# Kernel optimization log

Measured on AMD Instinct MI355X. Metric: run time of the kernel, lower is better.

The kernel has to match this reference:

```python
import jax, jax.numpy as jnp
import numpy as np

jax.config.update("jax_enable_x64", True)  # original uses complex128 FFTs

MS_H, MS_W, MS_D = 10, 10, 2
EPS = 1e-08


def _window_mean(x, wx, wy, wz):
    """Mean over all (wx,wy,wz) VALID windows of 3D x, via a summed-area table.
    Equivalent math to tf.nn.avg_pool3d(stride 1, VALID)."""
    X, Y, Z = x.shape
    A, B, C = X - wx + 1, Y - wy + 1, Z - wz + 1  # (2*MS_W+1, 2*MS_H+1, 2*MS_D+1)
    S = jnp.pad(jnp.cumsum(jnp.cumsum(jnp.cumsum(x, 0), 1), 2), ((1, 0), (1, 0), (1, 0)))
    g = lambda ox, oy, oz: jax.lax.dynamic_slice(S, (ox, oy, oz), (A, B, C))
    ws = (g(wx, wy, wz) - g(0, wy, wz) - g(wx, 0, wz) - g(wx, wy, 0)
          + g(0, 0, wz) + g(0, wy, 0) + g(wx, 0, 0) - g(0, 0, 0))
    return ws / float(wx * wy * wz)


def _forward(fr, template):
    # fr: (1, X, Y, Z, 1) float32; template: (X, Y, Z, 1) float32
    tpl = template[..., 0]                       # (X, Y, Z)
    X, Y, Z = tpl.shape
    # --- normalize_template ---
    tpl_zm = tpl - jnp.mean(tpl)
    tpl_var = jnp.sum(jnp.square(tpl_zm)) + EPS  # scalar
    target_freq = jnp.fft.fftn(tpl_zm.astype(jnp.complex128), axes=(0, 1, 2))
    # --- normalize_image ---
    img = fr[0, ..., 0]                          # (X, Y, Z)
    imgs_zm = img - jnp.mean(img)
    wx, wy, wz = X - 2 * MS_W, Y - 2 * MS_H, Z - 2 * MS_D
    m1 = _window_mean(img, wx, wy, wz)           # avg_pool3d of img
    m2 = _window_mean(jnp.square(img), wx, wy, wz)
    shp_prod = float(X * Y * Z)
    imgs_var = m2 - jnp.square(m1) / shp_prod + EPS
    imgs_var = jnp.where(imgs_var < 0, jnp.zeros_like(imgs_var), imgs_var)
    denominator = jnp.sqrt(tpl_var * imgs_var)   # (21, 21, 5)
    # --- FFT cross-correlation ---
    fr_freq = jnp.fft.fftn(imgs_zm.astype(jnp.complex128), axes=(0, 1, 2))
    cc = jnp.abs(jnp.fft.ifftn(fr_freq * jnp.conj(target_freq), axes=(0, 1, 2))).astype(jnp.float32)
    mx, my, mz = X // 2, Y // 2, Z // 2
    rolled_cc = jnp.roll(cc, (mx, my, mz), axis=(0, 1, 2))
    ncc = rolled_cc[mx - MS_W:mx + MS_W + 1,
                    my - MS_H:my + MS_H + 1,
                    mz - MS_D:mz + MS_D + 1] / denominator.astype(jnp.float32)
    ncc = jnp.where(jnp.isnan(ncc), jnp.zeros_like(ncc), ncc)
    # --- argmax_3d + Gaussian subpixel refine ---
    A, B, C = ncc.shape
    flat_idx = jnp.argmax(ncc.reshape(-1))
    sx = flat_idx // (B * C)
    sy = (flat_idx % (B * C)) // C
    sz = flat_idx - sx * (B * C) - C * sy
    ncc_log = jnp.log(ncc)
    v = lambda dx, dy, dz: ncc_log[sx + dx, sy + dy, sz + dz]
    six = 6.0 * v(0, 0, 0)
    sh_x = (-(sx - MS_H)).astype(jnp.float32) - (v(-1, 0, 0) - v(1, 0, 0)) / (2 * v(-1, 0, 0) - six + 2 * v(1, 0, 0))
    sh_y = (-(sy - MS_W)).astype(jnp.float32) - (v(0, -1, 0) - v(0, 1, 0)) / (2 * v(0, -1, 0) - six + 2 * v(0, 1, 0))
    sh_z = (-(sz - MS_D)).astype(jnp.float32) - (v(0, 0, -1) - v(0, 0, 1)) / (2 * v(0, 0, -1) - six + 2 * v(0, 0, 1))
    return (sh_x.reshape(1, 1), sh_y.reshape(1, 1), sh_z.reshape(1, 1),
            rolled_cc[None, ..., None], ncc[None, ..., None])


def setup_inputs() -> dict:
    key = jax.random.key(0)
    k1, k2 = jax.random.split(key)
    X, Y, Z = 512, 512, 32
    base = jax.random.normal(k1, (X, Y, Z), dtype=jnp.float32)
    # box-smooth so the NCC has a broad positive peak (log-interp stays finite)
    sm = base
    for ax in range(3):
        sm = sum(jnp.roll(sm, s, ax) for s in (-2, -1, 0, 1, 2)) / 5.0
    template = sm[..., None]
    fr = (jnp.roll(sm, (3, -2, 1), axis=(0, 1, 2))
          + 0.02 * jax.random.normal(k2, (X, Y, Z), dtype=jnp.float32))[None, ..., None]
    return {"fr": fr, "template": template}


def reference(fr, template):
    return _forward(fr, template)
```

## Files before the change

kernel.cpp:

```cpp
#include <hip/hip_runtime.h>
#include <hip/hip_bf16.h>
#include <math.h>


#define NTOT 8388608
#define NLINES 262144
#define OUT_ROLL_OFF 3
#define OUT_NCC_OFF 8388611
#define WIN_PROD 6777792.0
#define EPSV 1e-8

#define WS_HC_OFF 0UL
#define WS_ZS1_OFF 0UL
#define WS_ZS2_OFF 10485760UL
#define WS_YS1_OFF 20971520UL
#define WS_YS2_OFF 21401600UL
#define WS_PART_OFF 31457280UL
#define WS_DENOM_OFF 134217728UL

typedef float2 cf;
__device__ __forceinline__ cf cfadd(cf a, cf b){ return make_float2(a.x+b.x, a.y+b.y); }
__device__ __forceinline__ cf cfsub(cf a, cf b){ return make_float2(a.x-b.x, a.y-b.y); }
__device__ __forceinline__ cf cfmul(cf a, cf b){ return make_float2(a.x*b.x-a.y*b.y, a.x*b.y+a.y*b.x); }
__device__ __forceinline__ cf cfnegi(cf a){ return make_float2(a.y, -a.x); }
__device__ __forceinline__ cf cfposi(cf a){ return make_float2(-a.y, a.x); }

#define RT2F 0.70710678118654752440f
__device__ __forceinline__ cf cw64f(cf v){ return make_float2(RT2F*(v.x+v.y), RT2F*(v.y-v.x)); }
__device__ __forceinline__ cf cw192f(cf v){ return make_float2(RT2F*(v.y-v.x), -RT2F*(v.x+v.y)); }
__device__ __forceinline__ cf cw64i(cf v){ return make_float2(RT2F*(v.x-v.y), RT2F*(v.x+v.y)); }
__device__ __forceinline__ cf cw192i(cf v){ return make_float2(-RT2F*(v.x+v.y), RT2F*(v.x-v.y)); }

#define SKW(i) ((i) + ((i) >> 3))
#define LROW 580

template <int H>
__device__ __forceinline__ void fwd_r4(cf* ln, const cf* tw, int lane) {
    const int MUL2 = 256 / (2 * H);
#pragma unroll
    for (int g = 0; g < 2; ++g) {
        int j = lane + 64 * g;
        int t = j & (H - 1);
        int i0 = ((j & ~(H - 1)) << 2) + t;
        cf A = ln[SKW(i0)];
        cf B = ln[SKW(i0 + H)];
        cf C = ln[SKW(i0 + 2 * H)];
        cf D = ln[SKW(i0 + 3 * H)];
        cf w1 = tw[t * MUL2];
        cf w2 = make_float2(w1.x * w1.x - w1.y * w1.y, 2.0f * w1.x * w1.y);
        cf u = cfadd(A, C), v = cfadd(B, D);
        cf p = cfmul(cfsub(A, C), w1);
        cf q = cfnegi(cfmul(cfsub(B, D), w1));
        ln[SKW(i0)]         = cfadd(u, v);
        ln[SKW(i0 + H)]     = cfmul(cfsub(u, v), w2);
        ln[SKW(i0 + 2 * H)] = cfadd(p, q);
        ln[SKW(i0 + 3 * H)] = cfmul(cfsub(p, q), w2);
    }
}

template <int H>
__device__ __forceinline__ void inv_r4(cf* ln, const cf* tw, int lane) {
    const int MUL2 = 256 / (2 * H);
#pragma unroll
    for (int g = 0; g < 2; ++g) {
        int j = lane + 64 * g;
        int t = j & (H - 1);
        int i0 = ((j & ~(H - 1)) << 2) + t;
        cf A = ln[SKW(i0)];
        cf B = ln[SKW(i0 + H)];
        cf C = ln[SKW(i0 + 2 * H)];
        cf D = ln[SKW(i0 + 3 * H)];
        cf tww = tw[t * MUL2];
        cf w2 = make_float2(tww.x, -tww.y);
        cf wH = make_float2(w2.x * w2.x - w2.y * w2.y, 2.0f * w2.x * w2.y);
        cf vb = cfmul(B, wH), vd = cfmul(D, wH);
        cf a0 = cfadd(A, vb), a1 = cfsub(A, vb);
        cf c0 = cfadd(C, vd), c1 = cfsub(C, vd);
        cf t0 = cfmul(c0, w2);
        cf t1 = cfposi(cfmul(c1, w2));
        ln[SKW(i0)]         = cfadd(a0, t0);
        ln[SKW(i0 + 2 * H)] = cfsub(a0, t0);
        ln[SKW(i0 + H)]     = cfadd(a1, t1);
        ln[SKW(i0 + 3 * H)] = cfsub(a1, t1);
    }
}

__device__ __forceinline__ void fwd_r8(cf* ln, int lane) {
    cf* rp = ln + 9 * lane;
    cf L0 = rp[0], L1 = rp[1], L2 = rp[2], L3 = rp[3];
    cf L4 = rp[4], L5 = rp[5], L6 = rp[6], L7 = rp[7];
    cf s0 = cfadd(L0, L4), d0 = cfsub(L0, L4);
    cf s1 = cfadd(L1, L5), d1 = cw64f(cfsub(L1, L5));
    cf s2 = cfadd(L2, L6), d2 = cfnegi(cfsub(L2, L6));
    cf s3 = cfadd(L3, L7), d3 = cw192f(cfsub(L3, L7));
    cf e0 = cfadd(s0, s2), e2 = cfsub(s0, s2);
    cf e1 = cfadd(s1, s3), e3 = cfnegi(cfsub(s1, s3));
    cf f0 = cfadd(d0, d2), f2 = cfsub(d0, d2);
    cf f1 = cfadd(d1, d3), f3 = cfnegi(cfsub(d1, d3));
    rp[0] = cfadd(e0, e1); rp[1] = cfsub(e0, e1);
    rp[2] = cfadd(e2, e3); rp[3] = cfsub(e2, e3);
    rp[4] = cfadd(f0, f1); rp[5] = cfsub(f0, f1);
    rp[6] = cfadd(f2, f3); rp[7] = cfsub(f2, f3);
}

__device__ __forceinline__ void inv_r8(cf* ln, int lane) {
    cf* rp = ln + 9 * lane;
    cf L0 = rp[0], L1 = rp[1], L2 = rp[2], L3 = rp[3];
    cf L4 = rp[4], L5 = rp[5], L6 = rp[6], L7 = rp[7];
    cf a0 = cfadd(L0, L1), a1 = cfsub(L0, L1), a2 = cfadd(L2, L3), a3 = cfsub(L2, L3);
    cf a4 = cfadd(L4, L5), a5 = cfsub(L4, L5), a6 = cfadd(L6, L7), a7 = cfsub(L6, L7);
    cf b0 = cfadd(a0, a2), b2 = cfsub(a0, a2);
    cf v13 = cfposi(a3);
    cf b1 = cfadd(a1, v13), b3 = cfsub(a1, v13);
    cf b4 = cfadd(a4, a6), b6 = cfsub(a4, a6);
    cf v57 = cfposi(a7);
    cf b5 = cfadd(a5, v57), b7 = cfsub(a5, v57);
    cf v0 = b4, v1 = cw64i(b5), v2 = cfposi(b6), v3 = cw192i(b7);
    rp[0] = cfadd(b0, v0); rp[4] = cfsub(b0, v0);
    rp[1] = cfadd(b1, v1); rp[5] = cfsub(b1, v1);
    rp[2] = cfadd(b2, v2); rp[6] = cfsub(b2, v2);
    rp[3] = cfadd(b3, v3); rp[7] = cfsub(b3, v3);
}

template <int INV>
__device__ __forceinline__ void line_fft512(cf* ln, const cf* tw, int lane) {
    if (!INV) {
        fwd_r4<128>(ln, tw, lane);
        __builtin_amdgcn_wave_barrier();
        fwd_r4<32>(ln, tw, lane);
        __builtin_amdgcn_wave_barrier();
        fwd_r4<8>(ln, tw, lane);
        __builtin_amdgcn_wave_barrier();
        fwd_r8(ln, lane);
    } else {
        inv_r8(ln, lane);
        __builtin_amdgcn_wave_barrier();
        inv_r4<8>(ln, tw, lane);
        __builtin_amdgcn_wave_barrier();
        inv_r4<32>(ln, tw, lane);
        __builtin_amdgcn_wave_barrier();
        inv_r4<128>(ln, tw, lane);
    }
}

static constexpr float W32CF_[16] = {
    1.0f, 0.980785280403230449f, 0.923879532511286756f, 0.831469612302545237f,
    0.707106781186547524f, 0.555570233019602225f, 0.382683432365089772f, 0.195090322016128268f,
    0.0f, -0.195090322016128268f, -0.382683432365089772f, -0.555570233019602225f,
    -0.707106781186547524f, -0.831469612302545237f, -0.923879532511286756f, -0.980785280403230449f};
static constexpr float W32SF_[16] = {
    0.0f, 0.195090322016128268f, 0.382683432365089772f, 0.555570233019602225f,
    0.707106781186547524f, 0.831469612302545237f, 0.923879532511286756f, 0.980785280403230449f,
    1.0f, 0.980785280403230449f, 0.923879532511286756f, 0.831469612302545237f,
    0.707106781186547524f, 0.555570233019602225f, 0.382683432365089772f, 0.195090322016128268f};

template <int INV>
__device__ __forceinline__ void fft32(cf* a) {
    if (INV == 0) {
#pragma unroll
        for (int s = 0; s < 5; ++s) {
            const int h = 16 >> s;
#pragma unroll
            for (int j = 0; j < 16; ++j) {
                const int t = j & (h - 1);
                const int i0 = ((j >> (4 - s)) << (5 - s)) + t;
                const int i1 = i0 + h;
                cf u = a[i0], v = a[i1];
                a[i0] = make_float2(u.x + v.x, u.y + v.y);
                float dx = u.x - v.x, dy = u.y - v.y;
                const float wc = W32CF_[t << s];
                const float ws = -W32SF_[t << s];
                a[i1] = make_float2(dx * wc - dy * ws, dx * ws + dy * wc);
            }
        }
    } else {
#pragma unroll
        for (int s = 0; s < 5; ++s) {
            const int h = 1 << s;
#pragma unroll
            for (int j = 0; j < 16; ++j) {
                const int t = j & (h - 1);
                const int i0 = ((j >> s) << (s + 1)) + t;
                const int i1 = i0 + h;
                const float wc = W32CF_[t << (4 - s)];
                const float ws = W32SF_[t << (4 - s)];
                cf u = a[i0], vr = a[i1];
                cf v = make_float2(vr.x * wc - vr.y * ws, vr.x * ws + vr.y * wc);
                a[i0] = make_float2(u.x + v.x, u.y + v.y);
                a[i1] = make_float2(u.x - v.x, u.y - v.y);
            }
        }
    }
}

__device__ __forceinline__ int mir_br(int b) {
    if (b == 0) return 0;
    int s = 31 - __clz(b);
    return (3 << s) - 1 - b;
}

__global__ __launch_bounds__(256) void k_reduce_tpl(const float4* __restrict__ tpl4,
                                                    double2* __restrict__ part) {
    double st = 0, st2 = 0;
    const int stride = gridDim.x * blockDim.x;
    for (int i = blockIdx.x * blockDim.x + threadIdx.x; i < NTOT / 4; i += stride) {
        float4 t = tpl4[i];
        double t0 = t.x, t1 = t.y, t2 = t.z, t3 = t.w;
        st += t0 + t1 + t2 + t3;
        st2 += t0 * t0 + t1 * t1 + t2 * t2 + t3 * t3;
    }
    __shared__ double s1[256], s2[256];
    int tid = threadIdx.x;
    s1[tid] = st; s2[tid] = st2;
    __syncthreads();
    for (int s = 128; s > 0; s >>= 1) {
        if (tid < s) { s1[tid] += s1[tid + s]; s2[tid] += s2[tid + s]; }
        __syncthreads();
    }
    if (tid == 0) part[blockIdx.x] = make_double2(s1[0], s2[0]);
}

__global__ __launch_bounds__(256) void k_winz(const float* __restrict__ img,
                                              double* __restrict__ zs1,
                                              double* __restrict__ zs2) {
    int line = blockIdx.x * blockDim.x + threadIdx.x;
    long b = (long)line << 5;
    float v[32];
    const float4* p4 = (const float4*)(img + b);
#pragma unroll
    for (int q = 0; q < 8; ++q) {
        float4 f = p4[q];
        v[q * 4 + 0] = f.x; v[q * 4 + 1] = f.y; v[q * 4 + 2] = f.z; v[q * 4 + 3] = f.w;
    }
    double s1 = 0, s2 = 0;
#pragma unroll
    for (int z = 0; z < 28; ++z) {
        double t = (double)v[z];
        s1 += t;
        s2 += t * t;
    }
    long ob = (long)line * 5;
    zs1[ob] = s1; zs2[ob] = s2;
#pragma unroll
    for (int k = 1; k <= 4; ++k) {
        double a = (double)v[27 + k], r = (double)v[k - 1];
        s1 += a - r;
        s2 += a * a - r * r;
        zs1[ob + k] = s1; zs2[ob + k] = s2;
    }
}

__global__ __launch_bounds__(256) void k_winy(const double* __restrict__ zs1,
                                              const double* __restrict__ zs2,
                                              double* __restrict__ ys1,
                                              double* __restrict__ ys2) {
    int t = blockIdx.x * blockDim.x + threadIdx.x;
    if (t >= 2560) return;
    int x = t / 5, c = t % 5;
    long base = (long)x * 512 * 5 + c;
    double s1 = 0, s2 = 0;
    for (int y = 0; y < 492; ++y) {
        s1 += zs1[base + (long)y * 5];
        s2 += zs2[base + (long)y * 5];
    }
    long ob = (long)x * 105 + c;
    ys1[ob] = s1; ys2[ob] = s2;
    for (int k = 1; k <= 20; ++k) {
        s1 += zs1[base + (long)(491 + k) * 5] - zs1[base + (long)(k - 1) * 5];
        s2 += zs2[base + (long)(491 + k) * 5] - zs2[base + (long)(k - 1) * 5];
        ys1[ob + (long)k * 5] = s1;
        ys2[ob + (long)k * 5] = s2;
    }
}

__global__ __launch_bounds__(256) void k_winx_denom(const double* __restrict__ ys1,
                                                    const double* __restrict__ ys2,
                                                    const double2* __restrict__ part,
                                                    float* __restrict__ denom) {
    __shared__ double s1s[256], s2s[256];
    __shared__ double tplvar_s;
    int tid = threadIdx.x;
    {
        double a1 = 0, a2 = 0;
#pragma unroll
        for (int q = 0; q < 4; ++q) {
            double2 p = part[tid + 256 * q];
            a1 += p.x; a2 += p.y;
        }
        s1s[tid] = a1; s2s[tid] = a2;
        __syncthreads();
        for (int s = 128; s > 0; s >>= 1) {
            if (tid < s) { s1s[tid] += s1s[tid + s]; s2s[tid] += s2s[tid + s]; }
            __syncthreads();
        }
        if (tid == 0) {
            double S1 = s1s[0], S2 = s2s[0];
            double mu = S1 / (double)NTOT;
            tplvar_s = S2 - (double)NTOT * mu * mu + EPSV;
        }
        __syncthreads();
    }
    if (tid >= 105) return;
    const double tpl_var = tplvar_s;
    double s1 = 0, s2 = 0;
    for (int x = 0; x < 492; ++x) {
        s1 += ys1[(long)x * 105 + tid];
        s2 += ys2[(long)x * 105 + tid];
    }
    const double wm = 1.0 / WIN_PROD;
    for (int a = 0; a < 21; ++a) {
        double m1 = s1 * wm, m2 = s2 * wm;
        double iv = m2 - (m1 * m1) / (double)NTOT + EPSV;
        if (iv < 0) iv = 0;
        denom[a * 105 + tid] = (float)sqrt(tpl_var * iv);
        if (a < 20) {
            s1 += ys1[(long)(492 + a) * 105 + tid] - ys1[(long)a * 105 + tid];
            s2 += ys2[(long)(492 + a) * 105 + tid] - ys2[(long)a * 105 + tid];
        }
    }
}

__global__ __launch_bounds__(256) void k_pack_fft_z(const float* __restrict__ img,
                                                    const float* __restrict__ tpl,
                                                    cf* __restrict__ d) {
    int line = blockIdx.x * blockDim.x + threadIdx.x;
    long b = (long)line << 5;
    cf a[32];
    const float4* pi4 = (const float4*)(img + b);
    const float4* pt4 = (const float4*)(tpl + b);
#pragma unroll
    for (int q = 0; q < 8; ++q) {
        float4 fi = pi4[q];
        float4 ft = pt4[q];
        a[q * 4 + 0] = make_float2(fi.x, ft.x);
        a[q * 4 + 1] = make_float2(fi.y, ft.y);
        a[q * 4 + 2] = make_float2(fi.z, ft.z);
        a[q * 4 + 3] = make_float2(fi.w, ft.w);
    }
    fft32<0>(a);
#pragma unroll
    for (int z = 0; z < 32; ++z) d[b + z] = a[z];
}

template <int INV>
__global__ __launch_bounds__(1024, 8) void k_fft16(cf* __restrict__ d) {
    __shared__ cf ln[16][LROW];
    __shared__ cf tw[256];
    const int tid = threadIdx.x;
    if (tid < 256) {
        double sv, cv;
        sincos(6.283185307179586476925286766559 * (double)tid / 512.0, &sv, &cv);
        tw[tid] = make_float2((float)cv, (float)(-sv));
    }
    const long base = (long)(blockIdx.x >> 1) * 16384 + (blockIdx.x & 1) * 16;
#pragma unroll
    for (int i = 0; i < 8; ++i) {
        int idx = tid + 1024 * i;
        int lz = idx & 15, e = idx >> 4;
        ln[lz][SKW(e)] = d[base + (long)e * 32 + lz];
    }
    __syncthreads();
    const int c = tid >> 6, lane = tid & 63;
    line_fft512<INV>(ln[c], tw, lane);
    __syncthreads();
#pragma unroll
    for (int i = 0; i < 8; ++i) {
        int idx = tid + 1024 * i;
        int lz = idx & 15, e = idx >> 4;
        d[base + (long)e * 32 + lz] = ln[lz][SKW(e)];
    }
}

__global__ __launch_bounds__(1024, 8) void k_fftx_cross(cf* __restrict__ d) {
    const int bid = blockIdx.x;
    const int y = bid >> 2, tA = bid & 3;
    const int my = mir_br(y);
    const int tB = tA ^ (tA >> 1);
    const int keyA = (y << 2) | tA, keyB = (my << 2) | tB;
    if (keyA > keyB) return;
    const bool dup = (keyA == keyB);

    __shared__ cf ln[16][LROW];
    __shared__ cf tw[256];
    const int tid = threadIdx.x;
    if (tid < 256) {
        double sv, cv;
        sincos(6.283185307179586476925286766559 * (double)tid / 512.0, &sv, &cv);
        tw[tid] = make_float2((float)cv, (float)(-sv));
    }
    const int baseA = y * 32 + tA * 8;
    const int baseB = my * 32 + tB * 8;
#pragma unroll
    for (int i = 0; i < 8; ++i) {
        int idx = tid + 1024 * i;
        int a = idx & 7, half = (idx >> 3) & 1, bx = idx >> 4;
        ln[half * 8 + a][SKW(bx)] = d[(long)bx * 16384 + (half ? baseB : baseA) + a];
    }
    __syncthreads();
    const int c = tid >> 6, lane = tid & 63;
    line_fft512<0>(ln[c], tw, lane);
    __syncthreads();
    const bool dcblk = (bid == 0);
#pragma unroll
    for (int i = 0; i < 4; ++i) {
        int p = tid + 1024 * i;
        int a = p >> 9, bx = p & 511;
        int am = (tA == 0) ? mir_br(a) : 7 - a;
        int mbx = mir_br(bx);
        if (dcblk && p == 0) {
            ln[0][0] = make_float2(0.f, 0.f);
            ln[8][0] = make_float2(0.f, 0.f);
            continue;
        }
        cf h1 = ln[a][SKW(bx)];
        cf h2 = ln[8 + am][SKW(mbx)];
        float Fr = 0.5f * (h1.x + h2.x), Fi = 0.5f * (h1.y - h2.y);
        float Gr = 0.5f * (h1.y + h2.y), Gi = 0.5f * (h2.x - h1.x);
        float Pr = Fr * Gr + Fi * Gi;
        float Pi = Fi * Gr - Fr * Gi;
        ln[a][SKW(bx)] = make_float2(Pr, Pi);
        ln[8 + am][SKW(mbx)] = make_float2(Pr, -Pi);
    }
    __syncthreads();
    line_fft512<1>(ln[c], tw, lane);
    __syncthreads();
#pragma unroll
    for (int i = 0; i < 8; ++i) {
        int idx = tid + 1024 * i;
        int a = idx & 7, half = (idx >> 3) & 1, bx = idx >> 4;
        if (dup && half) continue;
        d[(long)bx * 16384 + (half ? baseB : baseA) + a] = ln[half * 8 + a][SKW(bx)];
    }
}

__global__ __launch_bounds__(256) void k_invz_abs_roll(const cf* __restrict__ d,
                                                       float* __restrict__ out) {
    int line = blockIdx.x * blockDim.x + threadIdx.x;
    int x = line >> 9, y = line & 511;
    long b = (long)line << 5;
    cf a[32];
#pragma unroll
    for (int z = 0; z < 32; ++z) a[z] = d[b + z];
    fft32<1>(a);
    const float invN = 1.0f / 8388608.0f;
    int xo = (x + 256) & 511, yo = (y + 256) & 511;
    long ob = OUT_ROLL_OFF + ((long)(xo << 9 | yo) << 5);
#pragma unroll
    for (int q = 0; q < 8; ++q) {
        int z = q * 4;
        int zo = (z + 16) & 31;
        float4 w;
        w.x = sqrtf(a[z + 0].x * a[z + 0].x + a[z + 0].y * a[z + 0].y) * invN;
        w.y = sqrtf(a[z + 1].x * a[z + 1].x + a[z + 1].y * a[z + 1].y) * invN;
        w.z = sqrtf(a[z + 2].x * a[z + 2].x + a[z + 2].y * a[z + 2].y) * invN;
        w.w = sqrtf(a[z + 3].x * a[z + 3].x + a[z + 3].y * a[z + 3].y) * invN;
        *(float4*)(out + ob + zo) = w;
    }
}

__global__ __launch_bounds__(256) void k_ncc_argmax(const float* __restrict__ denom,
                                                    float* __restrict__ out) {
    __shared__ float sncc[2205];
    __shared__ float bv[256];
    __shared__ int bi[256];
    const int tid = threadIdx.x;
    float best = -INFINITY;
    int bidx = 0x7fffffff;
    for (int i = tid; i < 2205; i += 256) {
        int a = i / 105, r = i % 105;
        int bq = r / 5, cq = r % 5;
        long ridx = OUT_ROLL_OFF + ((long)((246 + a) * 512 + (246 + bq)) << 5) + (14 + cq);
        float v = out[ridx] / denom[i];
        if (isnan(v)) v = 0.f;
        out[OUT_NCC_OFF + i] = v;
        sncc[i] = v;
        if (v > best) { best = v; bidx = i; }
    }
    bv[tid] = best;
    bi[tid] = bidx;
    __syncthreads();
    for (int s = 128; s > 0; s >>= 1) {
        if (tid < s) {
            if (bv[tid + s] > bv[tid] || (bv[tid + s] == bv[tid] && bi[tid + s] < bi[tid])) {
                bv[tid] = bv[tid + s];
                bi[tid] = bi[tid + s];
            }
        }
        __syncthreads();
    }
    if (tid == 0) {
        int idx = bi[0];
        int sx = idx / 105, sy = (idx % 105) / 5, sz = idx % 5;
        auto cl = [](int v, int n) { return v < 0 ? 0 : (v >= n ? n - 1 : v); };
        auto V = [&](int dx, int dy, int dz) {
            return logf(sncc[cl(sx + dx, 21) * 105 + cl(sy + dy, 21) * 5 + cl(sz + dz, 5)]);
        };
        float v0 = V(0, 0, 0);
        float six = 6.0f * v0;
        float am = V(-1, 0, 0), ap = V(1, 0, 0);
        float bm = V(0, -1, 0), bp = V(0, 1, 0);
        float cm = V(0, 0, -1), cp = V(0, 0, 1);
        out[0] = (float)(-(sx - 10)) - (am - ap) / (2.f * am - six + 2.f * ap);
        out[1] = (float)(-(sy - 10)) - (bm - bp) / (2.f * bm - six + 2.f * bp);
        out[2] = (float)(-(sz - 2)) - (cm - cp) / (2.f * cm - six + 2.f * cp);
    }
}

extern "C" void kernel_launch(void* const* d_in, const int* in_sizes, int n_in,
                              void* d_out, int out_size, void* d_ws, size_t ws_size,
                              hipStream_t stream) {
    const float* fr = (const float*)d_in[0];
    const float* tpl = (const float*)d_in[1];
    float* out = (float*)d_out;
    char* ws = (char*)d_ws;

    cf* Hc = (cf*)(ws + WS_HC_OFF);
    double* zs1 = (double*)(ws + WS_ZS1_OFF);
    double* zs2 = (double*)(ws + WS_ZS2_OFF);
    double* ys1 = (double*)(ws + WS_YS1_OFF);
    double* ys2 = (double*)(ws + WS_YS2_OFF);
    double2* part = (double2*)(ws + WS_PART_OFF);
    float* denom = (float*)(ws + WS_DENOM_OFF);

    k_reduce_tpl<<<1024, 256, 0, stream>>>((const float4*)tpl, part);
    k_winz<<<NLINES / 256, 256, 0, stream>>>(fr, zs1, zs2);
    k_winy<<<10, 256, 0, stream>>>(zs1, zs2, ys1, ys2);
    k_winx_denom<<<1, 256, 0, stream>>>(ys1, ys2, part, denom);

    k_pack_fft_z<<<NLINES / 256, 256, 0, stream>>>(fr, tpl, Hc);
    k_fft16<0><<<1024, 1024, 0, stream>>>(Hc);

    k_fftx_cross<<<2048, 1024, 0, stream>>>(Hc);

    k_fft16<1><<<1024, 1024, 0, stream>>>(Hc);
    k_invz_abs_roll<<<NLINES / 256, 256, 0, stream>>>(Hc, out);

    k_ncc_argmax<<<1, 256, 0, stream>>>(denom, out);
}
```

Baseline: 403.5 us.

## Fuse template stats, window z-sums and z-FFT pack into one pass

```diff
diff --git a/kernel.cpp b/kernel.cpp
--- a/kernel.cpp
+++ b/kernel.cpp
@@ -11,12 +11,12 @@
 #define EPSV 1e-8
 
 #define WS_HC_OFF 0UL
-#define WS_ZS1_OFF 0UL
-#define WS_ZS2_OFF 10485760UL
-#define WS_YS1_OFF 20971520UL
-#define WS_YS2_OFF 21401600UL
-#define WS_PART_OFF 31457280UL
-#define WS_DENOM_OFF 134217728UL
+#define WS_ZS1_OFF 67108864UL
+#define WS_ZS2_OFF 77594624UL
+#define WS_YS1_OFF 88080384UL
+#define WS_YS2_OFF 88510464UL
+#define WS_PART_OFF 88940544UL
+#define WS_DENOM_OFF 88957952UL
 
 typedef float2 cf;
 __device__ __forceinline__ cf cfadd(cf a, cf b){ return make_float2(a.x+b.x, a.y+b.y); }
@@ -199,55 +199,63 @@
     return (3 << s) - 1 - b;
 }
 
-__global__ __launch_bounds__(256) void k_reduce_tpl(const float4* __restrict__ tpl4,
+__global__ __launch_bounds__(256) void k_pack_stats(const float* __restrict__ img,
+                                                    const float* __restrict__ tpl,
+                                                    cf* __restrict__ d,
+                                                    double* __restrict__ zs1,
+                                                    double* __restrict__ zs2,
                                                     double2* __restrict__ part) {
-    double st = 0, st2 = 0;
-    const int stride = gridDim.x * blockDim.x;
-    for (int i = blockIdx.x * blockDim.x + threadIdx.x; i < NTOT / 4; i += stride) {
-        float4 t = tpl4[i];
-        double t0 = t.x, t1 = t.y, t2 = t.z, t3 = t.w;
-        st += t0 + t1 + t2 + t3;
-        st2 += t0 * t0 + t1 * t1 + t2 * t2 + t3 * t3;
-    }
-    __shared__ double s1[256], s2[256];
-    int tid = threadIdx.x;
-    s1[tid] = st; s2[tid] = st2;
-    __syncthreads();
-    for (int s = 128; s > 0; s >>= 1) {
-        if (tid < s) { s1[tid] += s1[tid + s]; s2[tid] += s2[tid + s]; }
-        __syncthreads();
-    }
-    if (tid == 0) part[blockIdx.x] = make_double2(s1[0], s2[0]);
-}
-
-__global__ __launch_bounds__(256) void k_winz(const float* __restrict__ img,
-                                              double* __restrict__ zs1,
-                                              double* __restrict__ zs2) {
     int line = blockIdx.x * blockDim.x + threadIdx.x;
     long b = (long)line << 5;
-    float v[32];
-    const float4* p4 = (const float4*)(img + b);
+    cf a[32];
+    const float4* pi4 = (const float4*)(img + b);
+    const float4* pt4 = (const float4*)(tpl + b);
 #pragma unroll
     for (int q = 0; q < 8; ++q) {
-        float4 f = p4[q];
-        v[q * 4 + 0] = f.x; v[q * 4 + 1] = f.y; v[q * 4 + 2] = f.z; v[q * 4 + 3] = f.w;
-    }
-    double s1 = 0, s2 = 0;
-#pragma unroll
-    for (int z = 0; z < 28; ++z) {
-        double t = (double)v[z];
-        s1 += t;
-        s2 += t * t;
-    }
-    long ob = (long)line * 5;
-    zs1[ob] = s1; zs2[ob] = s2;
-#pragma unroll
-    for (int k = 1; k <= 4; ++k) {
-        double a = (double)v[27 + k], r = (double)v[k - 1];
-        s1 += a - r;
-        s2 += a * a - r * r;
-        zs1[ob + k] = s1; zs2[ob + k] = s2;
-    }
+        float4 fi = pi4[q];
+        float4 ft = pt4[q];
+        a[q * 4 + 0] = make_float2(fi.x, ft.x);
+        a[q * 4 + 1] = make_float2(fi.y, ft.y);
+        a[q * 4 + 2] = make_float2(fi.z, ft.z);
+        a[q * 4 + 3] = make_float2(fi.w, ft.w);
+    }
+    {
+        double s1 = 0, s2 = 0;
+#pragma unroll
+        for (int z = 0; z < 28; ++z) {
+            double t = (double)a[z].x;
+            s1 += t; s2 += t * t;
+        }
+        long ob = (long)line * 5;
+        zs1[ob] = s1; zs2[ob] = s2;
+#pragma unroll
+        for (int k = 1; k <= 4; ++k) {
+            double ad = (double)a[27 + k].x, r = (double)a[k - 1].x;
+            s1 += ad - r;
+            s2 += ad * ad - r * r;
+            zs1[ob + k] = s1; zs2[ob + k] = s2;
+        }
+    }
+    {
+        double st = 0, st2 = 0;
+#pragma unroll
+        for (int z = 0; z < 32; ++z) {
+            double t = (double)a[z].y;
+            st += t; st2 += t * t;
+        }
+        __shared__ double r1[256], r2[256];
+        int tid = threadIdx.x;
+        r1[tid] = st; r2[tid] = st2;
+        __syncthreads();
+        for (int s = 128; s > 0; s >>= 1) {
+            if (tid < s) { r1[tid] += r1[tid + s]; r2[tid] += r2[tid + s]; }
+            __syncthreads();
+        }
+        if (tid == 0) part[blockIdx.x] = make_double2(r1[0], r2[0]);
+    }
+    fft32<0>(a);
+#pragma unroll
+    for (int z = 0; z < 32; ++z) d[b + z] = a[z];
 }
 
 __global__ __launch_bounds__(256) void k_winy(const double* __restrict__ zs1,
@@ -320,28 +328,6 @@
     }
 }
 
-__global__ __launch_bounds__(256) void k_pack_fft_z(const float* __restrict__ img,
-                                                    const float* __restrict__ tpl,
-                                                    cf* __restrict__ d) {
-    int line = blockIdx.x * blockDim.x + threadIdx.x;
-    long b = (long)line << 5;
-    cf a[32];
-    const float4* pi4 = (const float4*)(img + b);
-    const float4* pt4 = (const float4*)(tpl + b);
-#pragma unroll
-    for (int q = 0; q < 8; ++q) {
-        float4 fi = pi4[q];
-        float4 ft = pt4[q];
-        a[q * 4 + 0] = make_float2(fi.x, ft.x);
-        a[q * 4 + 1] = make_float2(fi.y, ft.y);
-        a[q * 4 + 2] = make_float2(fi.z, ft.z);
-        a[q * 4 + 3] = make_float2(fi.w, ft.w);
-    }
-    fft32<0>(a);
-#pragma unroll
-    for (int z = 0; z < 32; ++z) d[b + z] = a[z];
-}
-
 template <int INV>
 __global__ __launch_bounds__(1024, 8) void k_fft16(cf* __restrict__ d) {
     __shared__ cf ln[16][LROW];
@@ -371,16 +357,14 @@
     }
 }
 
-__global__ __launch_bounds__(1024, 8) void k_fftx_cross(cf* __restrict__ d) {
+__global__ __launch_bounds__(1024, 4) void k_fftx_cross(cf* __restrict__ d) {
     const int bid = blockIdx.x;
-    const int y = bid >> 2, tA = bid & 3;
+    const int y = bid >> 1, tile = bid & 1;
     const int my = mir_br(y);
-    const int tB = tA ^ (tA >> 1);
-    const int keyA = (y << 2) | tA, keyB = (my << 2) | tB;
-    if (keyA > keyB) return;
-    const bool dup = (keyA == keyB);
-
-    __shared__ cf ln[16][LROW];
+    if (y > my) return;
+    const bool dup = (y == my);
+
+    __shared__ cf ln[32][LROW];
     __shared__ cf tw[256];
     const int tid = threadIdx.x;
     if (tid < 256) {
@@ -388,48 +372,50 @@
         sincos(6.283185307179586476925286766559 * (double)tid / 512.0, &sv, &cv);
         tw[tid] = make_float2((float)cv, (float)(-sv));
     }
-    const int baseA = y * 32 + tA * 8;
-    const int baseB = my * 32 + tB * 8;
-#pragma unroll
-    for (int i = 0; i < 8; ++i) {
+    const int baseA = y * 32 + tile * 16;
+    const int baseB = my * 32 + tile * 16;
+#pragma unroll
+    for (int i = 0; i < 16; ++i) {
         int idx = tid + 1024 * i;
-        int a = idx & 7, half = (idx >> 3) & 1, bx = idx >> 4;
-        ln[half * 8 + a][SKW(bx)] = d[(long)bx * 16384 + (half ? baseB : baseA) + a];
+        int lz = idx & 15, half = (idx >> 4) & 1, bx = idx >> 5;
+        ln[half * 16 + lz][SKW(bx)] = d[(long)bx * 16384 + (half ? baseB : baseA) + lz];
     }
     __syncthreads();
     const int c = tid >> 6, lane = tid & 63;
     line_fft512<0>(ln[c], tw, lane);
+    line_fft512<0>(ln[16 + c], tw, lane);
     __syncthreads();
     const bool dcblk = (bid == 0);
 #pragma unroll
-    for (int i = 0; i < 4; ++i) {
+    for (int i = 0; i < 8; ++i) {
         int p = tid + 1024 * i;
         int a = p >> 9, bx = p & 511;
-        int am = (tA == 0) ? mir_br(a) : 7 - a;
+        int am = (tile == 0) ? mir_br(a) : 15 - a;
         int mbx = mir_br(bx);
         if (dcblk && p == 0) {
             ln[0][0] = make_float2(0.f, 0.f);
-            ln[8][0] = make_float2(0.f, 0.f);
+            ln[16][0] = make_float2(0.f, 0.f);
             continue;
         }
         cf h1 = ln[a][SKW(bx)];
-        cf h2 = ln[8 + am][SKW(mbx)];
+        cf h2 = ln[16 + am][SKW(mbx)];
         float Fr = 0.5f * (h1.x + h2.x), Fi = 0.5f * (h1.y - h2.y);
         float Gr = 0.5f * (h1.y + h2.y), Gi = 0.5f * (h2.x - h1.x);
         float Pr = Fr * Gr + Fi * Gi;
         float Pi = Fi * Gr - Fr * Gi;
         ln[a][SKW(bx)] = make_float2(Pr, Pi);
-        ln[8 + am][SKW(mbx)] = make_float2(Pr, -Pi);
+        ln[16 + am][SKW(mbx)] = make_float2(Pr, -Pi);
     }
     __syncthreads();
     line_fft512<1>(ln[c], tw, lane);
-    __syncthreads();
-#pragma unroll
-    for (int i = 0; i < 8; ++i) {
+    line_fft512<1>(ln[16 + c], tw, lane);
+    __syncthreads();
+#pragma unroll
+    for (int i = 0; i < 16; ++i) {
         int idx = tid + 1024 * i;
-        int a = idx & 7, half = (idx >> 3) & 1, bx = idx >> 4;
+        int lz = idx & 15, half = (idx >> 4) & 1, bx = idx >> 5;
         if (dup && half) continue;
-        d[(long)bx * 16384 + (half ? baseB : baseA) + a] = ln[half * 8 + a][SKW(bx)];
+        d[(long)bx * 16384 + (half ? baseB : baseA) + lz] = ln[half * 16 + lz][SKW(bx)];
     }
 }
 
@@ -439,8 +425,13 @@
     int x = line >> 9, y = line & 511;
     long b = (long)line << 5;
     cf a[32];
-#pragma unroll
-    for (int z = 0; z < 32; ++z) a[z] = d[b + z];
+    const float4* p4 = (const float4*)(d + b);
+#pragma unroll
+    for (int q = 0; q < 16; ++q) {
+        float4 f = p4[q];
+        a[2 * q]     = make_float2(f.x, f.y);
+        a[2 * q + 1] = make_float2(f.z, f.w);
+    }
     fft32<1>(a);
     const float invN = 1.0f / 8388608.0f;
     int xo = (x + 256) & 511, yo = (y + 256) & 511;
@@ -522,15 +513,14 @@
     double2* part = (double2*)(ws + WS_PART_OFF);
     float* denom = (float*)(ws + WS_DENOM_OFF);
 
-    k_reduce_tpl<<<1024, 256, 0, stream>>>((const float4*)tpl, part);
-    k_winz<<<NLINES / 256, 256, 0, stream>>>(fr, zs1, zs2);
+    k_pack_stats<<<NLINES / 256, 256, 0, stream>>>(fr, tpl, Hc, zs1, zs2, part);
+
     k_winy<<<10, 256, 0, stream>>>(zs1, zs2, ys1, ys2);
     k_winx_denom<<<1, 256, 0, stream>>>(ys1, ys2, part, denom);
 
-    k_pack_fft_z<<<NLINES / 256, 256, 0, stream>>>(fr, tpl, Hc);
     k_fft16<0><<<1024, 1024, 0, stream>>>(Hc);
 
-    k_fftx_cross<<<2048, 1024, 0, stream>>>(Hc);
+    k_fftx_cross<<<1024, 1024, 0, stream>>>(Hc);
 
     k_fft16<1><<<1024, 1024, 0, stream>>>(Hc);
     k_invz_abs_roll<<<NLINES / 256, 256, 0, stream>>>(Hc, out);
```

Result: faster. 392.9 us (-2.6%).
